# Kernel tuning notes

Measured on AMD Instinct MI355X. Metric: run time of the kernel, lower is better.

The kernel has to match this reference:

```python
import jax, jax.numpy as jnp
import numpy as np

B, N_TOK, DIM = 4, 16384, 256
NH, NP = 8, 4
HD = DIM // NH  # 32


def setup_inputs() -> dict:
    key = jax.random.key(0)
    ks = jax.random.split(key, 6)
    s = 0.02
    x = jax.random.normal(ks[0], (B, N_TOK, DIM), jnp.float32)
    v_w = jax.random.normal(ks[1], (DIM, DIM), jnp.float32) * s
    v_b = jnp.zeros((DIM,), jnp.float32)
    aw_w = jax.random.normal(ks[2], (NH * NP, DIM), jnp.float32) * s
    aw_b = jnp.zeros((NH * NP,), jnp.float32)
    # offsets: weight init to zeros, bias init per _reset_parameters
    off_w = jnp.zeros((NH * NP * 2, DIM), jnp.float32)
    thetas = np.arange(NH, dtype=np.float64) * (2.0 * np.pi / NH)
    g = np.stack([np.cos(thetas), np.sin(thetas)], -1)
    g = g / np.abs(g).max(-1, keepdims=True)
    g = np.tile(g[:, None, :], (1, NP, 1)) * np.arange(1, NP + 1)[None, :, None]
    off_b = jnp.asarray(g.reshape(-1), jnp.float32)
    proj_w = jax.random.normal(ks[3], (DIM, DIM), jnp.float32) * s
    proj_b = jnp.zeros((DIM,), jnp.float32)
    return dict(x=x, v_w=v_w, v_b=v_b, aw_w=aw_w, aw_b=aw_b,
                off_w=off_w, off_b=off_b, proj_w=proj_w, proj_b=proj_b,
                H=128, W=128)


def _grad_scale(t, scale):
    sg = jax.lax.stop_gradient(t)
    return sg + scale * (t - sg)


def _bilinear_point_attn(v, grid, weight):
    # v: [G, H, W, D] feature maps; grid: [G, N, P, 2] pixel coords (x, y);
    # weight: [G, N, P]. Zero padding outside the map (MSDeformAttn-style).
    G, Hh, Ww, D = v.shape
    gx, gy = grid[..., 0], grid[..., 1]
    x0 = jnp.floor(gx); y0 = jnp.floor(gy)
    wx1 = gx - x0; wx0 = 1.0 - wx1
    wy1 = gy - y0; wy0 = 1.0 - wy1
    x0i = x0.astype(jnp.int32); y0i = y0.astype(jnp.int32)
    v_flat = v.reshape(G, Hh * Ww, D)

    def gather(xi, yi):
        valid = ((xi >= 0) & (xi < Ww) & (yi >= 0) & (yi < Hh))
        xi_c = jnp.clip(xi, 0, Ww - 1)
        yi_c = jnp.clip(yi, 0, Hh - 1)
        idx = (yi_c * Ww + xi_c).reshape(G, -1, 1)
        g = jnp.take_along_axis(v_flat, idx, axis=1).reshape(*xi.shape, D)
        return g * valid[..., None].astype(v.dtype)

    g00 = gather(x0i, y0i)
    g10 = gather(x0i + 1, y0i)
    g01 = gather(x0i, y0i + 1)
    g11 = gather(x0i + 1, y0i + 1)
    samp = ((wy0 * wx0)[..., None] * g00 + (wy0 * wx1)[..., None] * g10
            + (wy1 * wx0)[..., None] * g01 + (wy1 * wx1)[..., None] * g11)
    # softmax-weighted aggregation over points
    return jnp.einsum('gnpd,gnp->gnd', samp, weight)


def reference(x, v_w, v_b, aw_w, aw_b, off_w, off_b, proj_w, proj_b, H, W):
    Bb, N, C = x.shape
    # v projection -> per-head feature maps [B*nh, H, W, hd]
    v = (x @ v_w.T + v_b).reshape(Bb, N, NH, HD)
    v = v.transpose(0, 2, 1, 3).reshape(Bb * NH, H, W, HD)
    # reference points: (x=col, y=row) pixel coords, shape [1, N, 1, 2]
    mh, mw = jnp.meshgrid(jnp.arange(H, dtype=x.dtype), jnp.arange(W, dtype=x.dtype), indexing='ij')
    ref_points = jnp.stack([mw, mh], -1).reshape(1, N, 1, 2)
    # offsets [B*nh, N, P, 2]
    offsets = (x @ off_w.T + off_b).reshape(Bb, N, NH, NP, 2)
    offsets = offsets.transpose(0, 2, 1, 3, 4).reshape(Bb * NH, N, NP, 2)
    grid = _grad_scale(ref_points + offsets, 0.1)
    # attention weights [B*nh, N, P], softmax over points
    w = (x @ aw_w.T + aw_b).reshape(Bb, N, NH, NP)
    w = w.transpose(0, 2, 1, 3).reshape(Bb * NH, N, NP)
    w = jax.nn.softmax(w, axis=-1)
    out = _bilinear_point_attn(v, grid, w)  # [B*nh, N, hd]
    out = out.reshape(Bb, NH, N, HD).transpose(0, 2, 1, 3).reshape(Bb, N, C)
    return out @ proj_w.T + proj_b
```

## Files before the change

### kernel.cpp

```cpp
#include <hip/hip_runtime.h>


typedef __attribute__((ext_vector_type(8))) short bf16x8;
typedef __attribute__((ext_vector_type(4))) float f32x4;

__device__ __forceinline__ short f2bf(float f) {
  unsigned u = __float_as_uint(f);
  u = u + 0x7FFFu + ((u >> 16) & 1u);
  return (short)(u >> 16);
}
__device__ __forceinline__ float bf2f(short s) {
  return __uint_as_float(((unsigned)(unsigned short)s) << 16);
}

__device__ __forceinline__ void gload16(const void* g, void* l) {
  __builtin_amdgcn_global_load_lds(
      (const __attribute__((address_space(1))) unsigned int*)g,
      (__attribute__((address_space(3))) unsigned int*)l, 16, 0, 0);
}

__global__ __launch_bounds__(256) void k_prep(
    const float* __restrict__ v_w, const float* __restrict__ aw_w,
    const float* __restrict__ off_w, const float* __restrict__ proj_w,
    short* __restrict__ wcat, short* __restrict__ wproj)
{
  int idx = blockIdx.x * 256 + threadIdx.x;
  if (idx < 384 * 256) {
    int row = idx >> 8;
    float val = 0.f;
    if (row < 256)      val = v_w[idx];
    else if (row < 288) val = aw_w[idx - 256 * 256];
    else if (row < 352) val = off_w[idx - 288 * 256];
    wcat[idx] = f2bf(val);
  } else {
    int j = idx - 384 * 256;
    wproj[j] = f2bf(proj_w[j]);
  }
}

__global__ __launch_bounds__(512, 4) void k_proj(
    const float* __restrict__ x, const short* __restrict__ wcat,
    const float* __restrict__ v_b, const float* __restrict__ aw_b,
    const float* __restrict__ off_b,
    unsigned short* __restrict__ vbuf,
    float* __restrict__ wts,
    float* __restrict__ offraw)
{
  __shared__ short Bs[96 * 256];
  const int tid  = threadIdx.x;
  const int wave = tid >> 6, lane = tid & 63;
  const int cp   = blockIdx.y;
  const int by   = blockIdx.x;
  const int cpb  = cp * 96;

#pragma unroll
  for (int i = 0; i < 6; ++i) {
    int f   = i * 512 + tid;
    int col = f >> 5, s = f & 31;
    int g   = (s & 24) | ((s & 7) ^ (col & 7));
    const short* src = wcat + (size_t)(cpb + col) * 256 + (g << 3);
    gload16(src, &Bs[(i * 512 + (wave << 6)) << 3]);
  }
  __syncthreads();

  const int lr = lane & 15, kg = lane >> 4;

#pragma unroll
  for (int sl = 0; sl < 2; ++sl) {
    const int sr0 = (by << 9) + ((wave + (sl << 3)) << 5);
    f32x4 acc[2][6] = {};

#pragma unroll
    for (int ks = 0; ks < 8; ++ks) {
      bf16x8 a[2];
#pragma unroll
      for (int rf = 0; rf < 2; ++rf) {
        const float* ap = x + (size_t)(sr0 + (rf << 4) + lr) * 256 + (ks << 5) + (kg << 3);
        f32x4 f0 = *(const f32x4*)ap;
        f32x4 f1 = *(const f32x4*)(ap + 4);
        bf16x8 v;
#pragma unroll
        for (int j = 0; j < 4; ++j) { v[j] = f2bf(f0[j]); v[4 + j] = f2bf(f1[j]); }
        a[rf] = v;
      }
#pragma unroll
      for (int cf = 0; cf < 6; ++cf) {
        int col = (cf << 4) + lr;
        int g = (ks << 2) + kg;
        int s = (g & 24) | ((g & 7) ^ (col & 7));
        bf16x8 b = *(const bf16x8*)&Bs[(col << 8) + (s << 3)];
        acc[0][cf] = __builtin_amdgcn_mfma_f32_16x16x32_bf16(a[0], b, acc[0][cf], 0, 0, 0);
        acc[1][cf] = __builtin_amdgcn_mfma_f32_16x16x32_bf16(a[1], b, acc[1][cf], 0, 0, 0);
      }
    }

#pragma unroll
    for (int cf = 0; cf < 6; ++cf) {
      const int cbase = cpb + (cf << 4);
      if (cbase >= 352) continue;
#pragma unroll
      for (int rf = 0; rf < 2; ++rf) {
#pragma unroll
        for (int j = 0; j < 4; ++j) {
          int r = sr0 + (rf << 4) + (kg << 2) + j;
          int b_ = r >> 14, nn = r & 16383;
          float v = acc[rf][cf][j];
          if (cbase < 256) {
            int c = cbase + lr;
            int h = c >> 5, d = c & 31;
            float val = v + v_b[c];
            vbuf[(((size_t)((b_ << 3) + h) << 14) + nn) * 32 + d] = (unsigned short)f2bf(val);
          } else if (cbase < 288) {
            int q = cbase - 256 + lr;
            float val = v + aw_b[q];
            float mx = fmaxf(val, __shfl_xor(val, 1));
            mx = fmaxf(mx, __shfl_xor(mx, 2));
            float e = __expf(val - mx);
            float ssum = e + __shfl_xor(e, 1);
            ssum += __shfl_xor(ssum, 2);
            float w = __fdividef(e, ssum);
            int h = q >> 2, p = q & 3;
            wts[(((size_t)((b_ << 3) + h) << 14) + nn) * 4 + p] = w;
          } else {
            int q = cbase - 288 + lr;
            int h = q >> 3, rest = q & 7;
            offraw[(((size_t)((b_ << 3) + h) << 14) + nn) * 8 + rest] = v + off_b[q];
          }
        }
      }
    }
  }
}

__global__ __launch_bounds__(256) void k_sample(
    const unsigned short* __restrict__ vbuf, const float* __restrict__ wts,
    const float* __restrict__ offraw, unsigned short* __restrict__ attn)
{
  const int tid  = threadIdx.x;
  const int item = (blockIdx.x << 6) + (tid >> 2);
  const int q    = tid & 3;
  const int g = item >> 14, n = item & 16383;
  const float px = (float)(n & 127), py = (float)(n >> 7);

  f32x4 w4 = *(const f32x4*)(wts + (size_t)item * 4);
  const f32x4* opv = (const f32x4*)(offraw + (size_t)item * 8);
  f32x4 o0 = opv[0], o1 = opv[1];
  float wv[4]  = {w4[0], w4[1], w4[2], w4[3]};
  float oxs[4] = {o0[0], o0[2], o1[0], o1[2]};
  float oys[4] = {o0[1], o0[3], o1[1], o1[3]};

  const unsigned short* vg = vbuf + (((size_t)g) << 19) + (q << 3);
  float o[8] = {};
#pragma unroll
  for (int p = 0; p < 4; ++p) {
    float gx = px + oxs[p], gy = py + oys[p];
    float x0f = floorf(gx), y0f = floorf(gy);
    float wx1 = gx - x0f, wx0 = 1.f - wx1;
    float wy1 = gy - y0f, wy0 = 1.f - wy1;
    int x0 = (int)x0f, y0 = (int)y0f;
    bool xv0 = (unsigned)x0 < 128u, xv1 = (unsigned)(x0 + 1) < 128u;
    bool yv0 = (unsigned)y0 < 128u, yv1 = (unsigned)(y0 + 1) < 128u;
    const unsigned short* base = vg + (((y0 << 7) + x0) << 5);
    bf16x8 c00 = {}, c10 = {}, c01 = {}, c11 = {};
    if (xv0 & yv0) c00 = *(const bf16x8*)(base);
    if (xv1 & yv0) c10 = *(const bf16x8*)(base + 32);
    if (xv0 & yv1) c01 = *(const bf16x8*)(base + 4096);
    if (xv1 & yv1) c11 = *(const bf16x8*)(base + 4128);
    float w00 = wv[p] * (wy0 * wx0), w10 = wv[p] * (wy0 * wx1);
    float w01 = wv[p] * (wy1 * wx0), w11 = wv[p] * (wy1 * wx1);
#pragma unroll
    for (int j = 0; j < 8; ++j)
      o[j] += w00 * bf2f(c00[j]) + w10 * bf2f(c10[j])
            + w01 * bf2f(c01[j]) + w11 * bf2f(c11[j]);
  }
  int b_ = g >> 3, h = g & 7;
  bf16x8 pk;
#pragma unroll
  for (int j = 0; j < 8; ++j) pk[j] = f2bf(o[j]);
  *(bf16x8*)(attn + ((((size_t)b_ << 14) + n) << 8) + (h << 5) + (q << 3)) = pk;
}

__global__ __launch_bounds__(512, 4) void k_out(
    const unsigned short* __restrict__ attn, const short* __restrict__ wproj,
    const float* __restrict__ proj_b, float* __restrict__ out)
{
  __shared__ short Bs[128 * 256];
  const int tid  = threadIdx.x;
  const int wave = tid >> 6, lane = tid & 63;
  const int cp   = blockIdx.y;
  const int by   = blockIdx.x;
  const int cpb  = cp << 7;

#pragma unroll
  for (int i = 0; i < 8; ++i) {
    int f   = i * 512 + tid;
    int col = f >> 5, s = f & 31;
    int g   = (s & 24) | ((s & 7) ^ (col & 7));
    const short* src = wproj + (size_t)(cpb + col) * 256 + (g << 3);
    gload16(src, &Bs[(i * 512 + (wave << 6)) << 3]);
  }
  __syncthreads();

  const int lr = lane & 15, kg = lane >> 4;
  const int sr0 = (by << 8) + (wave << 5);

  f32x4 acc[2][8] = {};
#pragma unroll
  for (int ks = 0; ks < 8; ++ks) {
    bf16x8 a[2];
#pragma unroll
    for (int rf = 0; rf < 2; ++rf)
      a[rf] = *(const bf16x8*)((const short*)attn +
               (size_t)(sr0 + (rf << 4) + lr) * 256 + (ks << 5) + (kg << 3));
#pragma unroll
    for (int cf = 0; cf < 8; ++cf) {
      int col = (cf << 4) + lr;
      int g = (ks << 2) + kg;
      int s = (g & 24) | ((g & 7) ^ (col & 7));
      bf16x8 b = *(const bf16x8*)&Bs[(col << 8) + (s << 3)];
      acc[0][cf] = __builtin_amdgcn_mfma_f32_16x16x32_bf16(a[0], b, acc[0][cf], 0, 0, 0);
      acc[1][cf] = __builtin_amdgcn_mfma_f32_16x16x32_bf16(a[1], b, acc[1][cf], 0, 0, 0);
    }
  }

#pragma unroll
  for (int cf = 0; cf < 8; ++cf) {
    int c = cpb + (cf << 4) + lr;
    float pb = proj_b[c];
#pragma unroll
    for (int rf = 0; rf < 2; ++rf) {
#pragma unroll
      for (int j = 0; j < 4; ++j) {
        int r = sr0 + (rf << 4) + (kg << 2) + j;
        out[(size_t)r * 256 + c] = acc[rf][cf][j] + pb;
      }
    }
  }
}

extern "C" void kernel_launch(void* const* d_in, const int* in_sizes, int n_in,
                              void* d_out, int out_size, void* d_ws, size_t ws_size,
                              hipStream_t stream)
{
  const float* x      = (const float*)d_in[0];
  const float* v_w    = (const float*)d_in[1];
  const float* v_b    = (const float*)d_in[2];
  const float* aw_w   = (const float*)d_in[3];
  const float* aw_b   = (const float*)d_in[4];
  const float* off_w  = (const float*)d_in[5];
  const float* off_b  = (const float*)d_in[6];
  const float* proj_w = (const float*)d_in[7];
  const float* proj_b = (const float*)d_in[8];
  float* out = (float*)d_out;

  char* ws = (char*)d_ws;
  short* wcat   = (short*)(ws + 0);
  short* wproj  = (short*)(ws + 262144);
  float* wts    = (float*)(ws + 1048576);
  float* offraw = (float*)(ws + 9437184);
  unsigned short* attn = (unsigned short*)(ws + 26214400);
  unsigned short* vbuf = (unsigned short*)d_out;

  hipLaunchKernelGGL(k_prep,   dim3(640),      dim3(256), 0, stream,
                     v_w, aw_w, off_w, proj_w, wcat, wproj);
  hipLaunchKernelGGL(k_proj,   dim3(128, 4),   dim3(512), 0, stream,
                     x, wcat, v_b, aw_b, off_b, vbuf, wts, offraw);
  hipLaunchKernelGGL(k_sample, dim3(8192),     dim3(256), 0, stream,
                     vbuf, wts, offraw, attn);
  hipLaunchKernelGGL(k_out,    dim3(256, 2),   dim3(512), 0, stream,
                     attn, wproj, proj_b, out);
}
```

Baseline: 233.2 us.

## Pre-convert x to bf16 and shrink GEMM column tiles with A-prefetch

```diff
diff --git a/kernel.cpp b/kernel.cpp
--- a/kernel.cpp
+++ b/kernel.cpp
@@ -20,41 +20,53 @@
 }
 
 __global__ __launch_bounds__(256) void k_prep(
+    const float* __restrict__ x,
     const float* __restrict__ v_w, const float* __restrict__ aw_w,
     const float* __restrict__ off_w, const float* __restrict__ proj_w,
-    short* __restrict__ wcat, short* __restrict__ wproj)
-{
-  int idx = blockIdx.x * 256 + threadIdx.x;
-  if (idx < 384 * 256) {
-    int row = idx >> 8;
-    float val = 0.f;
-    if (row < 256)      val = v_w[idx];
-    else if (row < 288) val = aw_w[idx - 256 * 256];
-    else if (row < 352) val = off_w[idx - 288 * 256];
-    wcat[idx] = f2bf(val);
+    short* __restrict__ xbf, short* __restrict__ wcat, short* __restrict__ wproj)
+{
+  int b = blockIdx.x;
+  if (b < 8192) {
+    size_t t = ((size_t)b << 8) + threadIdx.x;
+    const f32x4* src = (const f32x4*)(x + (t << 3));
+    f32x4 f0 = src[0], f1 = src[1];
+    bf16x8 v;
+#pragma unroll
+    for (int j = 0; j < 4; ++j) { v[j] = f2bf(f0[j]); v[4 + j] = f2bf(f1[j]); }
+    *(bf16x8*)(xbf + (t << 3)) = v;
   } else {
-    int j = idx - 384 * 256;
-    wproj[j] = f2bf(proj_w[j]);
-  }
-}
-
-__global__ __launch_bounds__(512, 4) void k_proj(
-    const float* __restrict__ x, const short* __restrict__ wcat,
+    int idx = (b - 8192) * 256 + threadIdx.x;
+    if (idx < 384 * 256) {
+      int row = idx >> 8;
+      float val = 0.f;
+      if (row < 256)      val = v_w[idx];
+      else if (row < 288) val = aw_w[idx - 256 * 256];
+      else if (row < 352) val = off_w[idx - 288 * 256];
+      wcat[idx] = f2bf(val);
+    } else {
+      int j = idx - 384 * 256;
+      wproj[j] = f2bf(proj_w[j]);
+    }
+  }
+}
+
+__global__ __launch_bounds__(512) void k_proj(
+    const short* __restrict__ xbf, const short* __restrict__ wcat,
     const float* __restrict__ v_b, const float* __restrict__ aw_b,
     const float* __restrict__ off_b,
     unsigned short* __restrict__ vbuf,
     float* __restrict__ wts,
     float* __restrict__ offraw)
 {
-  __shared__ short Bs[96 * 256];
+  __shared__ short Bs[64 * 256];
   const int tid  = threadIdx.x;
   const int wave = tid >> 6, lane = tid & 63;
   const int cp   = blockIdx.y;
   const int by   = blockIdx.x;
-  const int cpb  = cp * 96;
-
-#pragma unroll
-  for (int i = 0; i < 6; ++i) {
+  const int cpb  = cp << 6;
+
+#pragma unroll
+  for (int i = 0; i < 4; ++i) {
     int f   = i * 512 + tid;
     int col = f >> 5, s = f & 31;
     int g   = (s & 24) | ((s & 7) ^ (col & 7));
@@ -64,68 +76,64 @@
   __syncthreads();
 
   const int lr = lane & 15, kg = lane >> 4;
-
-#pragma unroll
-  for (int sl = 0; sl < 2; ++sl) {
-    const int sr0 = (by << 9) + ((wave + (sl << 3)) << 5);
-    f32x4 acc[2][6] = {};
-
-#pragma unroll
-    for (int ks = 0; ks < 8; ++ks) {
-      bf16x8 a[2];
-#pragma unroll
-      for (int rf = 0; rf < 2; ++rf) {
-        const float* ap = x + (size_t)(sr0 + (rf << 4) + lr) * 256 + (ks << 5) + (kg << 3);
-        f32x4 f0 = *(const f32x4*)ap;
-        f32x4 f1 = *(const f32x4*)(ap + 4);
-        bf16x8 v;
-#pragma unroll
-        for (int j = 0; j < 4; ++j) { v[j] = f2bf(f0[j]); v[4 + j] = f2bf(f1[j]); }
-        a[rf] = v;
-      }
-#pragma unroll
-      for (int cf = 0; cf < 6; ++cf) {
-        int col = (cf << 4) + lr;
-        int g = (ks << 2) + kg;
-        int s = (g & 24) | ((g & 7) ^ (col & 7));
-        bf16x8 b = *(const bf16x8*)&Bs[(col << 8) + (s << 3)];
-        acc[0][cf] = __builtin_amdgcn_mfma_f32_16x16x32_bf16(a[0], b, acc[0][cf], 0, 0, 0);
-        acc[1][cf] = __builtin_amdgcn_mfma_f32_16x16x32_bf16(a[1], b, acc[1][cf], 0, 0, 0);
-      }
-    }
-
-#pragma unroll
-    for (int cf = 0; cf < 6; ++cf) {
-      const int cbase = cpb + (cf << 4);
-      if (cbase >= 352) continue;
-#pragma unroll
-      for (int rf = 0; rf < 2; ++rf) {
-#pragma unroll
-        for (int j = 0; j < 4; ++j) {
-          int r = sr0 + (rf << 4) + (kg << 2) + j;
-          int b_ = r >> 14, nn = r & 16383;
-          float v = acc[rf][cf][j];
-          if (cbase < 256) {
-            int c = cbase + lr;
-            int h = c >> 5, d = c & 31;
-            float val = v + v_b[c];
-            vbuf[(((size_t)((b_ << 3) + h) << 14) + nn) * 32 + d] = (unsigned short)f2bf(val);
-          } else if (cbase < 288) {
-            int q = cbase - 256 + lr;
-            float val = v + aw_b[q];
-            float mx = fmaxf(val, __shfl_xor(val, 1));
-            mx = fmaxf(mx, __shfl_xor(mx, 2));
-            float e = __expf(val - mx);
-            float ssum = e + __shfl_xor(e, 1);
-            ssum += __shfl_xor(ssum, 2);
-            float w = __fdividef(e, ssum);
-            int h = q >> 2, p = q & 3;
-            wts[(((size_t)((b_ << 3) + h) << 14) + nn) * 4 + p] = w;
-          } else {
-            int q = cbase - 288 + lr;
-            int h = q >> 3, rest = q & 7;
-            offraw[(((size_t)((b_ << 3) + h) << 14) + nn) * 8 + rest] = v + off_b[q];
-          }
+  const int sr0 = (by << 8) + (wave << 5);
+  const short* arow0 = xbf + (size_t)(sr0 + lr) * 256 + (kg << 3);
+  const short* arow1 = xbf + (size_t)(sr0 + 16 + lr) * 256 + (kg << 3);
+
+  f32x4 acc[2][4] = {};
+  bf16x8 a0 = *(const bf16x8*)arow0;
+  bf16x8 a1 = *(const bf16x8*)arow1;
+
+#pragma unroll
+  for (int ks = 0; ks < 8; ++ks) {
+    bf16x8 n0, n1;
+    if (ks < 7) {
+      n0 = *(const bf16x8*)(arow0 + ((ks + 1) << 5));
+      n1 = *(const bf16x8*)(arow1 + ((ks + 1) << 5));
+    }
+#pragma unroll
+    for (int cf = 0; cf < 4; ++cf) {
+      int col = (cf << 4) + lr;
+      int g = (ks << 2) + kg;
+      int s = (g & 24) | ((g & 7) ^ (col & 7));
+      bf16x8 b = *(const bf16x8*)&Bs[(col << 8) + (s << 3)];
+      acc[0][cf] = __builtin_amdgcn_mfma_f32_16x16x32_bf16(a0, b, acc[0][cf], 0, 0, 0);
+      acc[1][cf] = __builtin_amdgcn_mfma_f32_16x16x32_bf16(a1, b, acc[1][cf], 0, 0, 0);
+    }
+    if (ks < 7) { a0 = n0; a1 = n1; }
+  }
+
+#pragma unroll
+  for (int cf = 0; cf < 4; ++cf) {
+    const int cbase = cpb + (cf << 4);
+    if (cbase >= 352) continue;
+#pragma unroll
+    for (int rf = 0; rf < 2; ++rf) {
+#pragma unroll
+      for (int j = 0; j < 4; ++j) {
+        int r = sr0 + (rf << 4) + (kg << 2) + j;
+        int b_ = r >> 14, nn = r & 16383;
+        float v = acc[rf][cf][j];
+        if (cbase < 256) {
+          int c = cbase + lr;
+          int h = c >> 5, d = c & 31;
+          float val = v + v_b[c];
+          vbuf[(((size_t)((b_ << 3) + h) << 14) + nn) * 32 + d] = (unsigned short)f2bf(val);
+        } else if (cbase < 288) {
+          int q = cbase - 256 + lr;
+          float val = v + aw_b[q];
+          float mx = fmaxf(val, __shfl_xor(val, 1));
+          mx = fmaxf(mx, __shfl_xor(mx, 2));
+          float e = __expf(val - mx);
+          float ssum = e + __shfl_xor(e, 1);
+          ssum += __shfl_xor(ssum, 2);
+          float w = __fdividef(e, ssum);
+          int h = q >> 2, p = q & 3;
+          wts[(((size_t)((b_ << 3) + h) << 14) + nn) * 4 + p] = w;
+        } else {
+          int q = cbase - 288 + lr;
+          int h = q >> 3, rest = q & 7;
+          offraw[(((size_t)((b_ << 3) + h) << 14) + nn) * 8 + rest] = v + off_b[q];
         }
       }
     }
@@ -180,19 +188,19 @@
   *(bf16x8*)(attn + ((((size_t)b_ << 14) + n) << 8) + (h << 5) + (q << 3)) = pk;
 }
 
-__global__ __launch_bounds__(512, 4) void k_out(
+__global__ __launch_bounds__(512) void k_out(
     const unsigned short* __restrict__ attn, const short* __restrict__ wproj,
     const float* __restrict__ proj_b, float* __restrict__ out)
 {
-  __shared__ short Bs[128 * 256];
+  __shared__ short Bs[64 * 256];
   const int tid  = threadIdx.x;
   const int wave = tid >> 6, lane = tid & 63;
   const int cp   = blockIdx.y;
   const int by   = blockIdx.x;
-  const int cpb  = cp << 7;
-
-#pragma unroll
-  for (int i = 0; i < 8; ++i) {
+  const int cpb  = cp << 6;
+
+#pragma unroll
+  for (int i = 0; i < 4; ++i) {
     int f   = i * 512 + tid;
     int col = f >> 5, s = f & 31;
     int g   = (s & 24) | ((s & 7) ^ (col & 7));
@@ -203,28 +211,34 @@
 
   const int lr = lane & 15, kg = lane >> 4;
   const int sr0 = (by << 8) + (wave << 5);
-
-  f32x4 acc[2][8] = {};
+  const short* arow0 = (const short*)attn + (size_t)(sr0 + lr) * 256 + (kg << 3);
+  const short* arow1 = (const short*)attn + (size_t)(sr0 + 16 + lr) * 256 + (kg << 3);
+
+  f32x4 acc[2][4] = {};
+  bf16x8 a0 = *(const bf16x8*)arow0;
+  bf16x8 a1 = *(const bf16x8*)arow1;
+
 #pragma unroll
   for (int ks = 0; ks < 8; ++ks) {
-    bf16x8 a[2];
-#pragma unroll
-    for (int rf = 0; rf < 2; ++rf)
-      a[rf] = *(const bf16x8*)((const short*)attn +
-               (size_t)(sr0 + (rf << 4) + lr) * 256 + (ks << 5) + (kg << 3));
-#pragma unroll
-    for (int cf = 0; cf < 8; ++cf) {
+    bf16x8 n0, n1;
+    if (ks < 7) {
+      n0 = *(const bf16x8*)(arow0 + ((ks + 1) << 5));
+      n1 = *(const bf16x8*)(arow1 + ((ks + 1) << 5));
+    }
+#pragma unroll
+    for (int cf = 0; cf < 4; ++cf) {
       int col = (cf << 4) + lr;
       int g = (ks << 2) + kg;
       int s = (g & 24) | ((g & 7) ^ (col & 7));
       bf16x8 b = *(const bf16x8*)&Bs[(col << 8) + (s << 3)];
-      acc[0][cf] = __builtin_amdgcn_mfma_f32_16x16x32_bf16(a[0], b, acc[0][cf], 0, 0, 0);
-      acc[1][cf] = __builtin_amdgcn_mfma_f32_16x16x32_bf16(a[1], b, acc[1][cf], 0, 0, 0);
-    }
-  }
-
-#pragma unroll
-  for (int cf = 0; cf < 8; ++cf) {
+      acc[0][cf] = __builtin_amdgcn_mfma_f32_16x16x32_bf16(a0, b, acc[0][cf], 0, 0, 0);
+      acc[1][cf] = __builtin_amdgcn_mfma_f32_16x16x32_bf16(a1, b, acc[1][cf], 0, 0, 0);
+    }
+    if (ks < 7) { a0 = n0; a1 = n1; }
+  }
+
+#pragma unroll
+  for (int cf = 0; cf < 4; ++cf) {
     int c = cpb + (cf << 4) + lr;
     float pb = proj_b[c];
 #pragma unroll
@@ -258,15 +272,16 @@
   short* wproj  = (short*)(ws + 262144);
   float* wts    = (float*)(ws + 1048576);
   float* offraw = (float*)(ws + 9437184);
+  short* xbf = (short*)(ws + 26214400);
   unsigned short* attn = (unsigned short*)(ws + 26214400);
   unsigned short* vbuf = (unsigned short*)d_out;
 
-  hipLaunchKernelGGL(k_prep,   dim3(640),      dim3(256), 0, stream,
-                     v_w, aw_w, off_w, proj_w, wcat, wproj);
-  hipLaunchKernelGGL(k_proj,   dim3(128, 4),   dim3(512), 0, stream,
-                     x, wcat, v_b, aw_b, off_b, vbuf, wts, offraw);
+  hipLaunchKernelGGL(k_prep,   dim3(8832),     dim3(256), 0, stream,
+                     x, v_w, aw_w, off_w, proj_w, xbf, wcat, wproj);
+  hipLaunchKernelGGL(k_proj,   dim3(256, 6),   dim3(512), 0, stream,
+                     xbf, wcat, v_b, aw_b, off_b, vbuf, wts, offraw);
   hipLaunchKernelGGL(k_sample, dim3(8192),     dim3(256), 0, stream,
                      vbuf, wts, offraw, attn);
-  hipLaunchKernelGGL(k_out,    dim3(256, 2),   dim3(512), 0, stream,
+  hipLaunchKernelGGL(k_out,    dim3(256, 4),   dim3(512), 0, stream,
                      attn, wproj, proj_b, out);
 }
```

New measurement: 238.5 us. 1.02x slower.
